# Kernel optimization log

Hardware: AMD Instinct MI355X
Metric: run time of the kernel (lower is better)

## Reference

```python
import jax, jax.numpy as jnp
import numpy as np

N, DEG, F_IN, HID, OUT = 20000, 16, 128, 128, 64
E = N * DEG


def setup_inputs() -> dict:
    key = jax.random.key(0)
    ks = jax.random.split(key, 12)
    s = 0.05  # small init scale to keep activations stable
    x = jax.random.normal(ks[0], (N, F_IN), jnp.float32)
    # PyG LSTM aggregation requires edges sorted by destination; fixed degree DEG
    src = jax.random.randint(ks[1], (E,), 0, N, dtype=jnp.int32)
    dst = jnp.repeat(jnp.arange(N, dtype=jnp.int32), DEG)
    edge_index = jnp.stack([src, dst])  # [2, E]
    return {
        "x": x,
        "edge_index": edge_index,
        "lstm_Wih": jax.random.normal(ks[2], (4, 4 * HID, F_IN), jnp.float32) * s,
        "lstm_Whh": jax.random.normal(ks[3], (4, 4 * HID, HID), jnp.float32) * s,
        "lstm_bih": jax.random.normal(ks[4], (4, 4 * HID), jnp.float32) * s,
        "lstm_bhh": jax.random.normal(ks[5], (4, 4 * HID), jnp.float32) * s,
        "linl_W123": jax.random.normal(ks[6], (3, HID, HID), jnp.float32) * s,
        "linl_b123": jax.random.normal(ks[7], (3, HID), jnp.float32) * s,
        "linr_W123": jax.random.normal(ks[8], (3, HID, HID), jnp.float32) * s,
        "linl_W4": jax.random.normal(ks[9], (OUT, HID), jnp.float32) * s,
        "linl_b4": jax.random.normal(ks[10], (OUT,), jnp.float32) * s,
        "linr_W4": jax.random.normal(ks[11], (OUT, HID), jnp.float32) * s,
    }


def _lstm_last(msgs, Wih, Whh, bih, bhh):
    """Run an LSTM over the padded neighbor sequence, return h at last step.
    msgs: [n, deg, f]. Matches PyG LSTMAggregation (lstm(x)[0][:, -1])."""
    n = msgs.shape[0]
    H = Whh.shape[1]
    b = bih + bhh  # torch LSTM adds both biases

    def step(carry, xt):  # xt: [n, f]
        h, c = carry
        g = xt @ Wih.T + h @ Whh.T + b  # [n, 4H], gate order i,f,g,o
        i, f, gg, o = jnp.split(g, 4, axis=-1)
        c = jax.nn.sigmoid(f) * c + jax.nn.sigmoid(i) * jnp.tanh(gg)
        h = jax.nn.sigmoid(o) * jnp.tanh(c)
        return (h, c), None

    h0 = jnp.zeros((n, H), msgs.dtype)
    (h, _), _ = jax.lax.scan(step, (h0, h0), jnp.swapaxes(msgs, 0, 1))
    return h


def _sage_conv(x, src, Wih, Whh, bih, bhh, Wl, bl, Wr):
    """SAGEConv(aggr='lstm'): lin_l(lstm_agg(x_j)) + lin_r(x).
    Fixed degree + dst-sorted edges => to_dense_batch is a reshape."""
    n, f = x.shape
    msgs = x[src].reshape(n, DEG, f)  # gather neighbor (source) features
    agg = _lstm_last(msgs, Wih, Whh, bih, bhh)
    return agg @ Wl.T + bl + x @ Wr.T  # lin_r has no bias in PyG


def reference(x, edge_index, lstm_Wih, lstm_Whh, lstm_bih, lstm_bhh,
              linl_W123, linl_b123, linr_W123, linl_W4, linl_b4, linr_W4):
    src = edge_index[0]
    # eval mode: dropout is identity
    x1 = jax.nn.relu(_sage_conv(x, src, lstm_Wih[0], lstm_Whh[0], lstm_bih[0],
                                lstm_bhh[0], linl_W123[0], linl_b123[0], linr_W123[0]))
    x2 = jax.nn.relu(_sage_conv(x1, src, lstm_Wih[1], lstm_Whh[1], lstm_bih[1],
                                lstm_bhh[1], linl_W123[1], linl_b123[1], linr_W123[1]) + x1)
    x3 = jax.nn.relu(_sage_conv(x2, src, lstm_Wih[2], lstm_Whh[2], lstm_bih[2],
                                lstm_bhh[2], linl_W123[2], linl_b123[2], linr_W123[2]) + x2)
    x4 = _sage_conv(x3, src, lstm_Wih[3], lstm_Whh[3], lstm_bih[3], lstm_bhh[3],
                    linl_W4, linl_b4, linr_W4)
    return x4
```

## Files before the change

### kernel.cpp

```cpp
#include <hip/hip_runtime.h>


#define N_NODES 20000
#define DEG 16
#define NPB 80
#define RT 5
#define SWZ(m) ((((m) ^ ((m) >> 3)) & 7))

typedef __bf16 bf16x8 __attribute__((ext_vector_type(8)));
typedef float f32x4 __attribute__((ext_vector_type(4)));

__device__ inline unsigned short f2bf(float f) {
  unsigned u = __builtin_bit_cast(unsigned, f);
  u += 0x7fffu + ((u >> 16) & 1u);
  return (unsigned short)(u >> 16);
}
__device__ inline float fexp2(float x) {
#if __has_builtin(__builtin_amdgcn_exp2f)
  return __builtin_amdgcn_exp2f(x);
#else
  return exp2f(x);
#endif
}
__device__ inline float frcp(float x) {
#if __has_builtin(__builtin_amdgcn_rcpf)
  return __builtin_amdgcn_rcpf(x);
#else
  return 1.f / x;
#endif
}

__device__ inline void barrier_lds() {
  asm volatile("s_waitcnt lgkmcnt(0)\n\ts_barrier" ::: "memory");
}

__global__ __launch_bounds__(256) void prep_weights(
    const float* __restrict__ Wih, const float* __restrict__ Whh,
    const float* __restrict__ bih, const float* __restrict__ bhh,
    unsigned short* __restrict__ WihB, unsigned short* __restrict__ WhhB,
    float* __restrict__ bsum) {
  int tid = blockIdx.x * 256 + threadIdx.x;
  int gate = ((tid >> 5) & 511) >> 7;
  float s = (gate == 2) ? -2.88539008f : -1.44269504f;
  float4 a = *(const float4*)(Wih + tid * 4);
  ushort4 o;
  o.x = f2bf(a.x * s); o.y = f2bf(a.y * s); o.z = f2bf(a.z * s); o.w = f2bf(a.w * s);
  *(ushort4*)(WihB + tid * 4) = o;
  float4 b = *(const float4*)(Whh + tid * 4);
  ushort4 p;
  p.x = f2bf(b.x * s); p.y = f2bf(b.y * s); p.z = f2bf(b.z * s); p.w = f2bf(b.w * s);
  *(ushort4*)(WhhB + tid * 4) = p;
  if (tid < 2048) {
    int g2 = (tid & 511) >> 7;
    float s2 = (g2 == 2) ? -2.88539008f : -1.44269504f;
    bsum[tid] = s2 * (bih[tid] + bhh[tid]);
  }
}

__global__ __launch_bounds__(256) void cast_bf(
    const float* __restrict__ x, unsigned short* __restrict__ xb) {
  int tid = blockIdx.x * 256 + threadIdx.x;
  float4 v = *(const float4*)(x + tid * 4);
  ushort4 o;
  o.x = f2bf(v.x); o.y = f2bf(v.y); o.z = f2bf(v.z); o.w = f2bf(v.w);
  *(ushort4*)(xb + tid * 4) = o;
}

__global__ __launch_bounds__(512, 2) void lstm_fused(
    const unsigned short* __restrict__ xbf,
    const int* __restrict__ src,
    const unsigned short* __restrict__ WihB,
    const unsigned short* __restrict__ WhhB,
    const float* __restrict__ bsum,
    float* __restrict__ agg) {
  __shared__ __align__(16) unsigned char xsb[2][NPB * 256];
  __shared__ __align__(16) unsigned char hbuf[2][NPB * 256];
  __shared__ __align__(16) int idx_s[NPB * DEG];
  const int tid = threadIdx.x;
  const int lane = tid & 63, w = tid >> 6;
  const int l15 = lane & 15, l4 = lane >> 4;
  const int node0 = blockIdx.x * NPB;
  const int colb = w * 16 + l15;

#pragma unroll
  for (int i = 0; i < 3; ++i) {
    int task = tid + i * 512;
    if (task < NPB * DEG) {
      int node = task >> 4, t = task & 15;
      idx_s[t * NPB + node] = src[node0 * DEG + task];
    }
  }

  bf16x8 bwx[4][4], bwh[4][4];
  float bs[4];
#pragma unroll
  for (int g = 0; g < 4; ++g) {
#pragma unroll
    for (int kt = 0; kt < 4; ++kt) {
      bwx[g][kt] = *(const bf16x8*)(WihB + (g * 128 + colb) * 128 + kt * 32 + l4 * 8);
      bwh[g][kt] = *(const bf16x8*)(WhhB + (g * 128 + colb) * 128 + kt * 32 + l4 * 8);
    }
    bs[g] = bsum[g * 128 + colb];
  }
  barrier_lds();

  const int task0 = tid, task1 = tid + 512;
  const int row0s = task0 >> 4, ch0 = task0 & 15;
  const int row1s = task1 >> 4, ch1 = task1 & 15;
  const int task2 = tid + 1024;
  const bool p2 = task2 < NPB * 16;
  const int row2s = task2 >> 4, ch2 = task2 & 15;

  {
    uint4 v0 = *(const uint4*)(xbf + idx_s[row0s] * 128 + (ch0 ^ SWZ(row0s)) * 8);
    uint4 v1 = *(const uint4*)(xbf + idx_s[row1s] * 128 + (ch1 ^ SWZ(row1s)) * 8);
    *(uint4*)(&xsb[0][row0s * 256 + ch0 * 16]) = v0;
    *(uint4*)(&xsb[0][row1s * 256 + ch1 * 16]) = v1;
    if (p2) {
      uint4 v2 = *(const uint4*)(xbf + idx_s[row2s] * 128 + (ch2 ^ SWZ(row2s)) * 8);
      *(uint4*)(&xsb[0][row2s * 256 + ch2 * 16]) = v2;
    }
  }
  barrier_lds();

  float c[RT][4];
#pragma unroll
  for (int rt = 0; rt < RT; ++rt)
#pragma unroll
    for (int r = 0; r < 4; ++r) c[rt][r] = 0.f;

#pragma unroll 2
  for (int t = 0; t < 16; ++t) {
    uint4 xstg0, xstg1, xstg2;
    if (t < 15) {
      const int tb = (t + 1) * NPB;
      xstg0 = *(const uint4*)(xbf + idx_s[tb + row0s] * 128 + (ch0 ^ SWZ(row0s)) * 8);
      xstg1 = *(const uint4*)(xbf + idx_s[tb + row1s] * 128 + (ch1 ^ SWZ(row1s)) * 8);
      if (p2)
        xstg2 = *(const uint4*)(xbf + idx_s[tb + row2s] * 128 + (ch2 ^ SWZ(row2s)) * 8);
    }

    const unsigned char* xrb = xsb[t & 1];
    const unsigned char* hb = hbuf[(t + 1) & 1];
    unsigned char* hw = hbuf[t & 1];

#pragma unroll
    for (int rt = 0; rt < RT; ++rt) {
      f32x4 acc[4];
#pragma unroll
      for (int g = 0; g < 4; ++g) acc[g] = (f32x4){bs[g], bs[g], bs[g], bs[g]};

      const int m = rt * 16 + l15;
#pragma unroll
      for (int kt = 0; kt < 4; ++kt) {
        int byte = (m * 256 + kt * 64 + l4 * 16) ^ (SWZ(m) << 4);
        bf16x8 a = *(const bf16x8*)(xrb + byte);
#pragma unroll
        for (int g = 0; g < 4; ++g)
          acc[g] = __builtin_amdgcn_mfma_f32_16x16x32_bf16(a, bwx[g][kt], acc[g], 0, 0, 0);
      }
      if (t > 0) {
#pragma unroll
        for (int kt = 0; kt < 4; ++kt) {
          int byte = (m * 256 + kt * 64 + l4 * 16) ^ (SWZ(m) << 4);
          bf16x8 a = *(const bf16x8*)(hb + byte);
#pragma unroll
          for (int g = 0; g < 4; ++g)
            acc[g] = __builtin_amdgcn_mfma_f32_16x16x32_bf16(a, bwh[g][kt], acc[g], 0, 0, 0);
        }
      }

#pragma unroll
      for (int r = 0; r < 4; ++r) {
        float ig = frcp(1.f + fexp2(acc[0][r]));
        float fg = frcp(1.f + fexp2(acc[1][r]));
        float gg = 2.f * frcp(1.f + fexp2(acc[2][r])) - 1.f;
        float og = frcp(1.f + fexp2(acc[3][r]));
        float cn = fg * c[rt][r] + ig * gg;
        c[rt][r] = cn;
        float th = 2.f * frcp(1.f + fexp2(-2.88539008f * cn)) - 1.f;
        float hv = og * th;
        int mm = rt * 16 + l4 * 4 + r;
        if (t < 15) {
          int byte = (mm * 256 + colb * 2) ^ (SWZ(mm) << 4);
          *(__bf16*)(hw + byte) = (__bf16)hv;
        } else {
          agg[(node0 + mm) * 128 + colb] = hv;
        }
      }
    }

    if (t < 15) {
      unsigned char* xw = xsb[(t + 1) & 1];
      *(uint4*)(&xw[row0s * 256 + ch0 * 16]) = xstg0;
      *(uint4*)(&xw[row1s * 256 + ch1 * 16]) = xstg1;
      if (p2) *(uint4*)(&xw[row2s * 256 + ch2 * 16]) = xstg2;
      barrier_lds();
    }
  }
}

__global__ __launch_bounds__(256) void gemm_out(
    const float* __restrict__ A1,
    const float* __restrict__ A2,
    const float* __restrict__ Wl, const float* __restrict__ bl,
    const float* __restrict__ Wr,
    const float* __restrict__ resid,
    float* __restrict__ out,
    unsigned short* __restrict__ outbf,
    int NOUT, int do_relu, int Nrows) {
  __shared__ __align__(16) unsigned char As[64 * 512];
  const int tid = threadIdx.x;
  const int lane = tid & 63, w = tid >> 6;
  const int l15 = lane & 15, l4 = lane >> 4;
  const int row0 = blockIdx.x * 64;

#pragma unroll
  for (int i = 0; i < 16; ++i) {
    int flat = i * 1024 + tid * 4;
    int r = flat >> 8, c = flat & 255;
    int grow = row0 + r;
    float4 v;
    if (grow < Nrows)
      v = (c < 128) ? *(const float4*)(A1 + grow * 128 + c)
                    : *(const float4*)(A2 + grow * 128 + (c - 128));
    else
      v = make_float4(0.f, 0.f, 0.f, 0.f);
    ushort4 b;
    b.x = f2bf(v.x); b.y = f2bf(v.y); b.z = f2bf(v.z); b.w = f2bf(v.w);
    int byte = (r * 512 + c * 2) ^ ((r & 7) << 4);
    *(ushort4*)(As + byte) = b;
  }
  __syncthreads();

  const int colg = blockIdx.y * 64 + w * 16 + l15;
  bf16x8 bw[8];
#pragma unroll
  for (int kt = 0; kt < 8; ++kt) {
    const float* bp = (kt < 4) ? (Wl + colg * 128 + kt * 32 + l4 * 8)
                               : (Wr + colg * 128 + (kt - 4) * 32 + l4 * 8);
    float4 a = *(const float4*)bp;
    float4 b = *(const float4*)(bp + 4);
    bf16x8 v;
    v[0] = (__bf16)a.x; v[1] = (__bf16)a.y; v[2] = (__bf16)a.z; v[3] = (__bf16)a.w;
    v[4] = (__bf16)b.x; v[5] = (__bf16)b.y; v[6] = (__bf16)b.z; v[7] = (__bf16)b.w;
    bw[kt] = v;
  }

  f32x4 acc[4];
#pragma unroll
  for (int rt = 0; rt < 4; ++rt) acc[rt] = (f32x4){0.f, 0.f, 0.f, 0.f};

#pragma unroll
  for (int kt = 0; kt < 8; ++kt) {
#pragma unroll
    for (int rt = 0; rt < 4; ++rt) {
      int m = rt * 16 + l15;
      int byte = (m * 512 + kt * 64 + l4 * 16) ^ ((m & 7) << 4);
      bf16x8 af = *(const bf16x8*)(As + byte);
      acc[rt] = __builtin_amdgcn_mfma_f32_16x16x32_bf16(af, bw[kt], acc[rt], 0, 0, 0);
    }
  }

  const float bias = bl[colg];
#pragma unroll
  for (int rt = 0; rt < 4; ++rt)
#pragma unroll
    for (int r = 0; r < 4; ++r) {
      int grow = row0 + rt * 16 + l4 * 4 + r;
      if (grow < Nrows) {
        float v = acc[rt][r] + bias;
        if (resid) v += resid[grow * 128 + colg];
        if (do_relu) v = fmaxf(v, 0.f);
        out[grow * NOUT + colg] = v;
        if (outbf) outbf[grow * 128 + colg] = f2bf(v);
      }
    }
}

extern "C" void kernel_launch(void* const* d_in, const int* in_sizes, int n_in,
                              void* d_out, int out_size, void* d_ws, size_t ws_size,
                              hipStream_t stream) {
  const float* X = (const float*)d_in[0];
  const int* src = (const int*)d_in[1];
  const float* Wih = (const float*)d_in[2];
  const float* Whh = (const float*)d_in[3];
  const float* bih = (const float*)d_in[4];
  const float* bhh = (const float*)d_in[5];
  const float* Wl123 = (const float*)d_in[6];
  const float* bl123 = (const float*)d_in[7];
  const float* Wr123 = (const float*)d_in[8];
  const float* Wl4 = (const float*)d_in[9];
  const float* bl4 = (const float*)d_in[10];
  const float* Wr4 = (const float*)d_in[11];
  float* out = (float*)d_out;

  char* ws = (char*)d_ws;
  unsigned short* xbf = (unsigned short*)ws;
  float* agg = (float*)(ws + 5120000);
  float* xb0 = (float*)(ws + 15360000);
  float* xb1 = (float*)(ws + 25600000);
  unsigned short* WihB = (unsigned short*)(ws + 35840000);
  unsigned short* WhhB = (unsigned short*)(ws + 36364288);
  float* bsumW = (float*)(ws + 36888576);

  prep_weights<<<dim3(256), 256, 0, stream>>>(Wih, Whh, bih, bhh, WihB, WhhB, bsumW);
  cast_bf<<<dim3(2500), 256, 0, stream>>>(X, xbf);

  const float* xcur = X;
  for (int L = 0; L < 4; ++L) {
    lstm_fused<<<dim3(250), 512, 0, stream>>>(xbf, src, WihB + L * 65536,
                                              WhhB + L * 65536, bsumW + L * 512, agg);
    if (L < 3) {
      float* nxt = (L & 1) ? xb1 : xb0;
      gemm_out<<<dim3(313, 2), 256, 0, stream>>>(agg, xcur, Wl123 + L * 16384,
                                                 bl123 + L * 128, Wr123 + L * 16384,
                                                 (L >= 1) ? xcur : nullptr, nxt, xbf,
                                                 128, 1, N_NODES);
      xcur = nxt;
    } else {
      gemm_out<<<dim3(313, 1), 256, 0, stream>>>(agg, xcur, Wl4, bl4, Wr4, nullptr, out,
                                                 nullptr, 64, 0, N_NODES);
    }
  }
}
```

Before: 451.1 us.

## Split LSTM waves into interleaved and batched MFMA/activation schedules

Waves in the fused LSTM kernel are split into two groups by a swizzled wave index. One group keeps the per-row-tile MFMA-then-activation order. The other issues all five row tiles' MFMAs first and then runs all activations. The goal is to have MFMA-heavy and transcendental-heavy phases from different waves overlap on the same SIMD. The batched path keeps 20 accumulator vectors live, which raises register pressure under a launch bound of 512 threads at 2 blocks, and it doubles code size.

Measured after the change: 1.159 ms. +156.8%, slower.

```diff
diff --git a/kernel.cpp b/kernel.cpp
--- a/kernel.cpp
+++ b/kernel.cpp
@@ -66,6 +66,56 @@
   *(ushort4*)(xb + tid * 4) = o;
 }
 
+#define ACT_BLOCK(ACC, RTI)                                               \
+  {                                                                       \
+    _Pragma("unroll")                                                     \
+    for (int r = 0; r < 4; ++r) {                                         \
+      float ig = frcp(1.f + fexp2(ACC[0][r]));                            \
+      float fg = frcp(1.f + fexp2(ACC[1][r]));                            \
+      float gg = 2.f * frcp(1.f + fexp2(ACC[2][r])) - 1.f;                \
+      float og = frcp(1.f + fexp2(ACC[3][r]));                            \
+      float cn = fg * c[RTI][r] + ig * gg;                                \
+      c[RTI][r] = cn;                                                     \
+      float th = 2.f * frcp(1.f + fexp2(-2.88539008f * cn)) - 1.f;        \
+      float hv = og * th;                                                 \
+      int mm = (RTI) * 16 + l4 * 4 + r;                                   \
+      if (t < 15) {                                                       \
+        int byte = (mm * 256 + colb * 2) ^ (SWZ(mm) << 4);                \
+        *(__bf16*)(hw + byte) = (__bf16)hv;                               \
+      } else {                                                            \
+        agg[(node0 + mm) * 128 + colb] = hv;                              \
+      }                                                                   \
+    }                                                                     \
+  }
+
+#define XPART(ACC, RTI)                                                   \
+  {                                                                       \
+    const int m = (RTI) * 16 + l15;                                       \
+    _Pragma("unroll")                                                     \
+    for (int kt = 0; kt < 4; ++kt) {                                      \
+      int byte = (m * 256 + kt * 64 + l4 * 16) ^ (SWZ(m) << 4);           \
+      bf16x8 a = *(const bf16x8*)(xrb + byte);                            \
+      _Pragma("unroll")                                                   \
+      for (int g = 0; g < 4; ++g)                                         \
+        ACC[g] = __builtin_amdgcn_mfma_f32_16x16x32_bf16(a, bwx[g][kt],   \
+                                                         ACC[g], 0, 0, 0);\
+    }                                                                     \
+  }
+
+#define HPART(ACC, RTI)                                                   \
+  {                                                                       \
+    const int m = (RTI) * 16 + l15;                                       \
+    _Pragma("unroll")                                                     \
+    for (int kt = 0; kt < 4; ++kt) {                                      \
+      int byte = (m * 256 + kt * 64 + l4 * 16) ^ (SWZ(m) << 4);           \
+      bf16x8 a = *(const bf16x8*)(hb + byte);                             \
+      _Pragma("unroll")                                                   \
+      for (int g = 0; g < 4; ++g)                                         \
+        ACC[g] = __builtin_amdgcn_mfma_f32_16x16x32_bf16(a, bwh[g][kt],   \
+                                                         ACC[g], 0, 0, 0);\
+    }                                                                     \
+  }
+
 __global__ __launch_bounds__(512, 2) void lstm_fused(
     const unsigned short* __restrict__ xbf,
     const int* __restrict__ src,
@@ -81,6 +131,7 @@
   const int l15 = lane & 15, l4 = lane >> 4;
   const int node0 = blockIdx.x * NPB;
   const int colb = w * 16 + l15;
+  const int pgrp = (w ^ (w >> 2)) & 1;
 
 #pragma unroll
   for (int i = 0; i < 3; ++i) {
@@ -129,73 +180,74 @@
 #pragma unroll
     for (int r = 0; r < 4; ++r) c[rt][r] = 0.f;
 
+  if (pgrp == 0) {
 #pragma unroll 2
-  for (int t = 0; t < 16; ++t) {
-    uint4 xstg0, xstg1, xstg2;
-    if (t < 15) {
-      const int tb = (t + 1) * NPB;
-      xstg0 = *(const uint4*)(xbf + idx_s[tb + row0s] * 128 + (ch0 ^ SWZ(row0s)) * 8);
-      xstg1 = *(const uint4*)(xbf + idx_s[tb + row1s] * 128 + (ch1 ^ SWZ(row1s)) * 8);
-      if (p2)
-        xstg2 = *(const uint4*)(xbf + idx_s[tb + row2s] * 128 + (ch2 ^ SWZ(row2s)) * 8);
-    }
-
-    const unsigned char* xrb = xsb[t & 1];
-    const unsigned char* hb = hbuf[(t + 1) & 1];
-    unsigned char* hw = hbuf[t & 1];
-
-#pragma unroll
-    for (int rt = 0; rt < RT; ++rt) {
-      f32x4 acc[4];
-#pragma unroll
-      for (int g = 0; g < 4; ++g) acc[g] = (f32x4){bs[g], bs[g], bs[g], bs[g]};
-
-      const int m = rt * 16 + l15;
-#pragma unroll
-      for (int kt = 0; kt < 4; ++kt) {
-        int byte = (m * 256 + kt * 64 + l4 * 16) ^ (SWZ(m) << 4);
-        bf16x8 a = *(const bf16x8*)(xrb + byte);
-#pragma unroll
-        for (int g = 0; g < 4; ++g)
-          acc[g] = __builtin_amdgcn_mfma_f32_16x16x32_bf16(a, bwx[g][kt], acc[g], 0, 0, 0);
-      }
-      if (t > 0) {
-#pragma unroll
-        for (int kt = 0; kt < 4; ++kt) {
-          int byte = (m * 256 + kt * 64 + l4 * 16) ^ (SWZ(m) << 4);
-          bf16x8 a = *(const bf16x8*)(hb + byte);
-#pragma unroll
-          for (int g = 0; g < 4; ++g)
-            acc[g] = __builtin_amdgcn_mfma_f32_16x16x32_bf16(a, bwh[g][kt], acc[g], 0, 0, 0);
-        }
-      }
-
-#pragma unroll
-      for (int r = 0; r < 4; ++r) {
-        float ig = frcp(1.f + fexp2(acc[0][r]));
-        float fg = frcp(1.f + fexp2(acc[1][r]));
-        float gg = 2.f * frcp(1.f + fexp2(acc[2][r])) - 1.f;
-        float og = frcp(1.f + fexp2(acc[3][r]));
-        float cn = fg * c[rt][r] + ig * gg;
-        c[rt][r] = cn;
-        float th = 2.f * frcp(1.f + fexp2(-2.88539008f * cn)) - 1.f;
-        float hv = og * th;
-        int mm = rt * 16 + l4 * 4 + r;
-        if (t < 15) {
-          int byte = (mm * 256 + colb * 2) ^ (SWZ(mm) << 4);
-          *(__bf16*)(hw + byte) = (__bf16)hv;
-        } else {
-          agg[(node0 + mm) * 128 + colb] = hv;
-        }
-      }
-    }
-
-    if (t < 15) {
-      unsigned char* xw = xsb[(t + 1) & 1];
-      *(uint4*)(&xw[row0s * 256 + ch0 * 16]) = xstg0;
-      *(uint4*)(&xw[row1s * 256 + ch1 * 16]) = xstg1;
-      if (p2) *(uint4*)(&xw[row2s * 256 + ch2 * 16]) = xstg2;
-      barrier_lds();
+    for (int t = 0; t < 16; ++t) {
+      uint4 xstg0, xstg1, xstg2;
+      if (t < 15) {
+        const int tb = (t + 1) * NPB;
+        xstg0 = *(const uint4*)(xbf + idx_s[tb + row0s] * 128 + (ch0 ^ SWZ(row0s)) * 8);
+        xstg1 = *(const uint4*)(xbf + idx_s[tb + row1s] * 128 + (ch1 ^ SWZ(row1s)) * 8);
+        if (p2)
+          xstg2 = *(const uint4*)(xbf + idx_s[tb + row2s] * 128 + (ch2 ^ SWZ(row2s)) * 8);
+      }
+      const unsigned char* xrb = xsb[t & 1];
+      const unsigned char* hb = hbuf[(t + 1) & 1];
+      unsigned char* hw = hbuf[t & 1];
+
+#pragma unroll
+      for (int rt = 0; rt < RT; ++rt) {
+        f32x4 acc[4];
+#pragma unroll
+        for (int g = 0; g < 4; ++g) acc[g] = (f32x4){bs[g], bs[g], bs[g], bs[g]};
+        XPART(acc, rt)
+        if (t > 0) HPART(acc, rt)
+        ACT_BLOCK(acc, rt)
+      }
+
+      if (t < 15) {
+        unsigned char* xw = xsb[(t + 1) & 1];
+        *(uint4*)(&xw[row0s * 256 + ch0 * 16]) = xstg0;
+        *(uint4*)(&xw[row1s * 256 + ch1 * 16]) = xstg1;
+        if (p2) *(uint4*)(&xw[row2s * 256 + ch2 * 16]) = xstg2;
+        barrier_lds();
+      }
+    }
+  } else {
+#pragma unroll 2
+    for (int t = 0; t < 16; ++t) {
+      uint4 xstg0, xstg1, xstg2;
+      if (t < 15) {
+        const int tb = (t + 1) * NPB;
+        xstg0 = *(const uint4*)(xbf + idx_s[tb + row0s] * 128 + (ch0 ^ SWZ(row0s)) * 8);
+        xstg1 = *(const uint4*)(xbf + idx_s[tb + row1s] * 128 + (ch1 ^ SWZ(row1s)) * 8);
+        if (p2)
+          xstg2 = *(const uint4*)(xbf + idx_s[tb + row2s] * 128 + (ch2 ^ SWZ(row2s)) * 8);
+      }
+      const unsigned char* xrb = xsb[t & 1];
+      const unsigned char* hb = hbuf[(t + 1) & 1];
+      unsigned char* hw = hbuf[t & 1];
+
+      f32x4 acc5[RT][4];
+#pragma unroll
+      for (int rt = 0; rt < RT; ++rt) {
+#pragma unroll
+        for (int g = 0; g < 4; ++g) acc5[rt][g] = (f32x4){bs[g], bs[g], bs[g], bs[g]};
+        XPART(acc5[rt], rt)
+        if (t > 0) HPART(acc5[rt], rt)
+      }
+#pragma unroll
+      for (int rt = 0; rt < RT; ++rt) {
+        ACT_BLOCK(acc5[rt], rt)
+      }
+
+      if (t < 15) {
+        unsigned char* xw = xsb[(t + 1) & 1];
+        *(uint4*)(&xw[row0s * 256 + ch0 * 16]) = xstg0;
+        *(uint4*)(&xw[row1s * 256 + ch1 * 16]) = xstg1;
+        if (p2) *(uint4*)(&xw[row2s * 256 + ch2 * 16]) = xstg2;
+        barrier_lds();
+      }
     }
   }
 }
```
